# Optimization experiments

Hardware: AMD Instinct MI355X
Metric: run time of the kernel (lower is better)

The kernel has to match this reference:

```python
import jax, jax.numpy as jnp
import numpy as np

V, E, H, S, B, MAX_OOV = 50000, 256, 512, 500, 64, 50


def setup_inputs() -> dict:
    key = jax.random.key(0)
    ks = jax.random.split(key, 22)
    s = 0.02  # param init scale
    return {
        "input_token": jax.random.randint(ks[0], (B, 1), 0, V),
        "encoder_hidden_states": jax.random.normal(ks[1], (S, B, 2 * H), jnp.float32),
        "projected_encoder_hidden_states": jax.random.normal(ks[2], (S, B, H), jnp.float32),
        "src_mask": jnp.ones((B, S), dtype=bool),
        "prev_hidden": jax.random.normal(ks[3], (1, B, H), jnp.float32),
        "encoder_batch_extended_vocab": jax.random.randint(ks[4], (B, S), 0, V + MAX_OOV),
        "batch_max_oov": MAX_OOV,
        # learned parameters
        "emb": jax.random.normal(ks[5], (V, E), jnp.float32) * s,
        "attn_Wq": jax.random.normal(ks[6], (H, H), jnp.float32) * s,   # query_layer, no bias
        "attn_We": jax.random.normal(ks[7], (1, H), jnp.float32) * s,   # energy_layer, no bias
        "gru_Wih": jax.random.normal(ks[8], (3 * H, E + 2 * H), jnp.float32) * s,
        "gru_Whh": jax.random.normal(ks[9], (3 * H, H), jnp.float32) * s,
        "gru_bih": jax.random.normal(ks[10], (3 * H,), jnp.float32) * s,
        "gru_bhh": jax.random.normal(ks[11], (3 * H,), jnp.float32) * s,
        "lin_W": jax.random.normal(ks[12], (H, E + 3 * H), jnp.float32) * s,
        "lin_b": jax.random.normal(ks[13], (H,), jnp.float32) * s,
        "pg_W": jax.random.normal(ks[14], (1, E + 3 * H), jnp.float32) * s,
        "pg_b": jax.random.normal(ks[15], (1,), jnp.float32) * s,
        "out_W": jax.random.normal(ks[16], (V, H), jnp.float32) * s,
        "out_b": jax.random.normal(ks[17], (V,), jnp.float32) * s,
    }


def _forward(input_token, enc_h, proj_key, prev_hidden, ext_vocab, max_oov,
             emb, attn_Wq, attn_We, gru_Wih, gru_Whh, gru_bih, gru_bhh,
             lin_W, lin_b, pg_W, pg_b, out_W, out_b):
    b = input_token.shape[0]
    embed = jnp.transpose(emb[input_token], (1, 0, 2))  # [1,B,E]

    # Bahdanau attention (softmax over source dim 0; mask unused, as in source)
    q = jnp.einsum('tbh,oh->tbo', prev_hidden, attn_Wq)            # [1,B,H]
    scores = jnp.einsum('sbh,oh->sb', jnp.tanh(q + proj_key), attn_We)  # [S,B]
    alphas = jax.nn.softmax(scores, axis=0)                        # [S,B]
    context = jnp.einsum('sb,sbd->bd', alphas, enc_h)[None]        # [1,B,2H]
    attention_dist = alphas.T                                      # [B,S]

    # GRU cell (torch gate order: r, z, n)
    x = jnp.concatenate([embed, context], axis=2)[0]               # [B,E+2H]
    h = prev_hidden[0]                                             # [B,H]
    gi = x @ gru_Wih.T + gru_bih                                   # [B,3H]
    gh = h @ gru_Whh.T + gru_bhh
    i_r, i_z, i_n = jnp.split(gi, 3, axis=1)
    h_r, h_z, h_n = jnp.split(gh, 3, axis=1)
    r = jax.nn.sigmoid(i_r + h_r)
    z = jax.nn.sigmoid(i_z + h_z)
    n = jnp.tanh(i_n + r * h_n)
    h_new = (1.0 - z) * n + z * h                                  # [B,H]
    rnn_output = h_new[None]                                       # [1,B,H]

    concat = jnp.concatenate([embed, rnn_output, context], axis=2)  # [1,B,E+3H]
    p_gen = jax.nn.sigmoid(jnp.einsum('tbf,of->tbo', concat, pg_W) + pg_b)  # [1,B,1]
    lin = jnp.einsum('tbf,of->tbo', concat, lin_W) + lin_b          # [1,B,H]
    logits = jnp.einsum('tbh,vh->tbv', lin, out_W) + out_b          # [1,B,V]

    gen_prob = p_gen * jax.nn.softmax(logits, axis=2)               # [1,B,V]
    attn_prob = ((1.0 - p_gen) * attention_dist[None])[0]           # [B,S]

    ext = jnp.concatenate(
        [gen_prob, jnp.zeros((1, b, max_oov), gen_prob.dtype)], axis=2) + 1e-12  # [1,B,V+oov]
    rows = jnp.arange(b)[:, None]
    merged = ext.at[0, rows, ext_vocab].add(attn_prob)              # scatter_add over vocab dim
    output = jnp.log(merged)
    return output, h_new[None]


def reference(input_token, encoder_hidden_states, projected_encoder_hidden_states,
              src_mask, prev_hidden, encoder_batch_extended_vocab, batch_max_oov,
              emb, attn_Wq, attn_We, gru_Wih, gru_Whh, gru_bih, gru_bhh,
              lin_W, lin_b, pg_W, pg_b, out_W, out_b):
    return _forward(input_token, encoder_hidden_states, projected_encoder_hidden_states,
                    prev_hidden, encoder_batch_extended_vocab, batch_max_oov,
                    emb, attn_Wq, attn_We, gru_Wih, gru_Whh, gru_bih, gru_bhh,
                    lin_W, lin_b, pg_W, pg_b, out_W, out_b)
```

## Files before the change

### kernel.cpp

```cpp
#include <hip/hip_runtime.h>
#include <hip/hip_bf16.h>
#include <math.h>

namespace {
constexpr int V = 50000, E = 256, H = 512, S = 500, B = 64, OOVN = 50;
constexpr int VEXT = V + OOVN;
constexpr int CCAT = E + 3 * H;
constexpr int G3 = 3 * H;
constexpr int NLB = 391;

typedef __attribute__((ext_vector_type(8))) short short8;
typedef __attribute__((ext_vector_type(4))) float f32x4;

__device__ __forceinline__ float wsum(float v) {
#pragma unroll
  for (int off = 32; off > 0; off >>= 1) v += __shfl_xor(v, off, 64);
  return v;
}
__device__ __forceinline__ float sigmoidf(float x) { return 1.f / (1.f + __expf(-x)); }
__device__ __forceinline__ float fast_tanh(float x) {
  x = fminf(fmaxf(x, -15.f), 15.f);
  float e = __expf(2.f * x);
  return __fdividef(e - 1.f, e + 1.f);
}
__device__ __forceinline__ void smerge_s(float& m, float& l, float om, float ol) {
  float nm = fmaxf(m, om);
  if (nm == -INFINITY) { m = nm; return; }
  l = l * __expf(m - nm) + ol * __expf(om - nm);
  m = nm;
}
__device__ __forceinline__ short bf16_rn_s(float f) {
  __hip_bfloat16 h = __float2bfloat16(f);
  return __builtin_bit_cast(short, h);
}
__device__ __forceinline__ void hilo8(float4 a, float4 b, short8& hi, short8& lo) {
  float f[8] = {a.x, a.y, a.z, a.w, b.x, b.y, b.z, b.w};
#pragma unroll
  for (int i = 0; i < 8; ++i) {
    unsigned u = __float_as_uint(f[i]);
    hi[i] = (short)(u >> 16);
    lo[i] = bf16_rn_s(f[i] - __uint_as_float(u & 0xffff0000u));
  }
}

template <int KSTEPS>
__device__ __forceinline__ void gemm_core_f32(const float* __restrict__ X, int ldx,
                                              int xk0, const float* __restrict__ W,
                                              int ldw, int wk0, int n0, f32x4 acc[4]) {
  const int l = threadIdx.x & 63;
  const int r16 = l & 15, q16 = l >> 4;
#pragma unroll
  for (int t = 0; t < 4; ++t) acc[t] = (f32x4){0.f, 0.f, 0.f, 0.f};
  const float* wp = W + (size_t)(n0 + r16) * ldw + wk0 + q16 * 8;
  const float* xp[4];
#pragma unroll
  for (int t = 0; t < 4; ++t) xp[t] = X + (size_t)(t * 16 + r16) * ldx + xk0 + q16 * 8;
#pragma unroll
  for (int ks = 0; ks < KSTEPS; ++ks) {
    const int ko = ks * 32;
    float4 w0 = *reinterpret_cast<const float4*>(wp + ko);
    float4 w1 = *reinterpret_cast<const float4*>(wp + ko + 4);
    short8 whi, wlo;
    hilo8(w0, w1, whi, wlo);
#pragma unroll
    for (int t = 0; t < 4; ++t) {
      float4 x0 = *reinterpret_cast<const float4*>(xp[t] + ko);
      float4 x1 = *reinterpret_cast<const float4*>(xp[t] + ko + 4);
      short8 ah, al;
      hilo8(x0, x1, ah, al);
      acc[t] = __builtin_amdgcn_mfma_f32_16x16x32_bf16(ah, whi, acc[t], 0, 0, 0);
      acc[t] = __builtin_amdgcn_mfma_f32_16x16x32_bf16(al, whi, acc[t], 0, 0, 0);
      acc[t] = __builtin_amdgcn_mfma_f32_16x16x32_bf16(ah, wlo, acc[t], 0, 0, 0);
    }
  }
}
template <int KSTEPS>
__device__ __forceinline__ void gemm_store_f32(const float* X, int ldx, int xk0,
                                               const float* W, int ldw, int wk0, int n0,
                                               float* C, int ldc) {
  f32x4 acc[4];
  gemm_core_f32<KSTEPS>(X, ldx, xk0, W, ldw, wk0, n0, acc);
  const int l = threadIdx.x & 63;
  const int r16 = l & 15, q16 = l >> 4;
#pragma unroll
  for (int t = 0; t < 4; ++t)
#pragma unroll
    for (int r = 0; r < 4; ++r) {
      int row = t * 16 + q16 * 4 + r;
      C[(size_t)row * ldc + n0 + r16] = acc[t][r];
    }
}

__global__ void __launch_bounds__(256) k_head(const float* __restrict__ prevh,
                                              const float* __restrict__ Wq,
                                              const float* __restrict__ Whh,
                                              const int* __restrict__ tok,
                                              const float* __restrict__ emb,
                                              float* __restrict__ qpart,
                                              float* __restrict__ ghp,
                                              float* __restrict__ cc) {
  int gw = blockIdx.x * 4 + (threadIdx.x >> 6);
  if (gw < 128) {
    int c = gw >> 5, nt = gw & 31;
    gemm_store_f32<4>(prevh, H, c * 128, Wq, H, c * 128, nt * 16,
                      qpart + (size_t)c * 64 * H, H);
  } else if (gw < 320) {
    int w2 = gw - 128;
    int c = w2 / 96, nt = w2 % 96;
    gemm_store_f32<8>(prevh, H, c * 256, Whh, H, c * 256, nt * 16,
                      ghp + (size_t)c * 64 * G3, G3);
  } else {
    int idx = (gw - 320) * 64 + (threadIdx.x & 63);
    for (int i = idx; i < B * E; i += 1024) {
      int b = i >> 8, e = i & 255;
      cc[b * CCAT + e] = emb[(size_t)tok[b] * E + e];
    }
    for (int i = idx; i < B * 1024; i += 1024) {
      int b = i >> 10, col = i & 1023;
      cc[b * CCAT + 768 + col] = 0.f;
    }
  }
}

__global__ void k_scores(const float* __restrict__ qpart, const float* __restrict__ pk,
                         const float* __restrict__ We, float* __restrict__ scoresT) {
  int lane = threadIdx.x & 63;
  int gw = blockIdx.x * 4 + (threadIdx.x >> 6);
  int s = gw >> 6, b = gw & 63;
  const float* q0 = qpart + b * H + lane * 8;
  const float* kr = pk + ((size_t)s * B + b) * H + lane * 8;
  const float* er = We + lane * 8;
  float part = 0.f;
#pragma unroll
  for (int i = 0; i < 2; ++i) {
    float4 qa = *reinterpret_cast<const float4*>(q0 + i * 4);
    float4 qb = *reinterpret_cast<const float4*>(q0 + 64 * H + i * 4);
    float4 qc = *reinterpret_cast<const float4*>(q0 + 128 * H + i * 4);
    float4 qd = *reinterpret_cast<const float4*>(q0 + 192 * H + i * 4);
    float4 kv = *reinterpret_cast<const float4*>(kr + i * 4);
    float4 ev = *reinterpret_cast<const float4*>(er + i * 4);
    part += fast_tanh(qa.x + qb.x + qc.x + qd.x + kv.x) * ev.x +
            fast_tanh(qa.y + qb.y + qc.y + qd.y + kv.y) * ev.y +
            fast_tanh(qa.z + qb.z + qc.z + qd.z + kv.z) * ev.z +
            fast_tanh(qa.w + qb.w + qc.w + qd.w + kv.w) * ev.w;
  }
  part = wsum(part);
  if (lane == 0) scoresT[b * S + s] = part;
}

__global__ void k_softmax_s(const float* __restrict__ scoresT, float* __restrict__ alphasT) {
  int b = blockIdx.x, t = threadIdx.x;
  int w = t >> 6, lane = t & 63;
  __shared__ float rm[8], rl[8];
  float v = (t < S) ? scoresT[b * S + t] : -INFINITY;
  float m = v;
#pragma unroll
  for (int off = 32; off > 0; off >>= 1) m = fmaxf(m, __shfl_xor(m, off, 64));
  if (lane == 0) rm[w] = m;
  __syncthreads();
  float bm = rm[0];
#pragma unroll
  for (int i = 1; i < 8; ++i) bm = fmaxf(bm, rm[i]);
  float e = (t < S) ? __expf(v - bm) : 0.f;
  float sw = wsum(e);
  if (lane == 0) rl[w] = sw;
  __syncthreads();
  float tot = rl[0];
#pragma unroll
  for (int i = 1; i < 8; ++i) tot += rl[i];
  if (t < S) alphasT[b * S + t] = e / tot;
}

__global__ void k_ctx(const float* __restrict__ alphasT, const float* __restrict__ ench,
                      float* __restrict__ cc) {
  int x = blockIdx.x;
  int b = x >> 3, qd = (x >> 2) & 1 * 0 + ((x & 7) >> 1), sh = x & 1;
  int t = threadIdx.x;
  __shared__ float sa[250];
  if (t < 250) sa[t] = alphasT[b * S + sh * 250 + t];
  __syncthreads();
  const float* base = ench + ((size_t)(sh * 250) * B + b) * 1024 + qd * 256 + t;
  float a0 = 0.f, a1 = 0.f, a2 = 0.f, a3 = 0.f;
#pragma unroll 4
  for (int s = 0; s < 248; s += 4) {
    a0 += sa[s] * base[(size_t)s * (B * 1024)];
    a1 += sa[s + 1] * base[(size_t)(s + 1) * (B * 1024)];
    a2 += sa[s + 2] * base[(size_t)(s + 2) * (B * 1024)];
    a3 += sa[s + 3] * base[(size_t)(s + 3) * (B * 1024)];
  }
  a0 += sa[248] * base[(size_t)248 * (B * 1024)];
  a1 += sa[249] * base[(size_t)249 * (B * 1024)];
  atomicAdd(&cc[b * CCAT + 768 + qd * 256 + t], (a0 + a1) + (a2 + a3));
}

__global__ void __launch_bounds__(256) k_gemm_big(const float* __restrict__ cc,
                                                  const float* __restrict__ Wih,
                                                  const float* __restrict__ linW,
                                                  float* __restrict__ gip,
                                                  float* __restrict__ linpart) {
  int w = blockIdx.x * 4 + (threadIdx.x >> 6);
  if (w < 480) {
    int c = w / 96, nt = w % 96;
    int xk0 = (c == 0) ? 0 : 768 + (c - 1) * 256;
    gemm_store_f32<8>(cc, CCAT, xk0, Wih, 1280, c * 256, nt * 16,
                      gip + (size_t)c * 64 * G3, G3);
  } else {
    int w2 = w - 480;
    int c = w2 >> 5, nt = w2 & 31;
    int k0 = (c == 0) ? 0 : 768 + (c - 1) * 256;
    gemm_store_f32<8>(cc, CCAT, k0, linW, CCAT, k0, nt * 16,
                      linpart + (size_t)c * 64 * H, H);
  }
}

__global__ void k_gates(const float* __restrict__ gip, const float* __restrict__ ghp,
                        const float* __restrict__ bih, const float* __restrict__ bhh,
                        const float* __restrict__ prevh, const float* __restrict__ pgW,
                        const float* __restrict__ pgb, float* __restrict__ cc,
                        float* __restrict__ hout, float* __restrict__ pgsum) {
  int b = blockIdx.x, j = threadIdx.x;
  float ir = bih[j], iz = bih[512 + j], in_ = bih[1024 + j];
#pragma unroll
  for (int c = 0; c < 5; ++c) {
    const float* g = gip + (size_t)c * 64 * G3 + b * G3;
    ir += g[j]; iz += g[512 + j]; in_ += g[1024 + j];
  }
  float hr = bhh[j], hz = bhh[512 + j], hn = bhh[1024 + j];
#pragma unroll
  for (int c = 0; c < 2; ++c) {
    const float* g = ghp + (size_t)c * 64 * G3 + b * G3;
    hr += g[j]; hz += g[512 + j]; hn += g[1024 + j];
  }
  float r = sigmoidf(ir + hr);
  float z = sigmoidf(iz + hz);
  float n = fast_tanh(in_ + r * hn);
  float h = prevh[b * H + j];
  float hnew = (1.f - z) * n + z * h;
  hout[b * H + j] = hnew;
  cc[b * CCAT + E + j] = hnew;
  float acc = hnew * pgW[E + j];
  acc += cc[b * CCAT + 768 + j] * pgW[768 + j];
  acc += cc[b * CCAT + 1280 + j] * pgW[1280 + j];
  if (j < 256) acc += cc[b * CCAT + j] * pgW[j];
  acc = wsum(acc);
  __shared__ float sl[8];
  int w = j >> 6, lane = j & 63;
  if (lane == 0) sl[w] = acc;
  __syncthreads();
  if (j == 0) {
    float tot = pgb[0];
#pragma unroll
    for (int i = 0; i < 8; ++i) tot += sl[i];
    pgsum[b] = tot;
  }
}

__global__ void __launch_bounds__(256) k_linfin(const float* __restrict__ cc,
                                                const float* __restrict__ linW,
                                                const float* __restrict__ linpart,
                                                const float* __restrict__ linb,
                                                short* __restrict__ lh) {
  int w = blockIdx.x * 4 + (threadIdx.x >> 6);
  f32x4 acc[4];
  gemm_core_f32<16>(cc, CCAT, 256, linW, CCAT, 256, w * 16, acc);
  const int l = threadIdx.x & 63;
  const int r16 = l & 15, q16 = l >> 4;
  int col = w * 16 + r16;
  float bv = linb[col];
#pragma unroll
  for (int t = 0; t < 4; ++t)
#pragma unroll
    for (int r = 0; r < 4; ++r) {
      int row = t * 16 + q16 * 4 + r;
      float v = acc[t][r] + bv;
#pragma unroll
      for (int c = 0; c < 5; ++c) v += linpart[(size_t)c * 64 * H + row * H + col];
      lh[row * H + col] = bf16_rn_s(v);
    }
}

__global__ void __launch_bounds__(512) k_gemm_logits(
    const short* __restrict__ lh, const float* __restrict__ outW,
    const float* __restrict__ outb, float* __restrict__ logits,
    float* __restrict__ pm, float* __restrict__ pl) {
  __shared__ __align__(16) short xs[64 * 512];
  __shared__ float pml[8][64][2];
  char* xb = reinterpret_cast<char*>(xs);
  int tid = threadIdx.x;
#pragma unroll
  for (int k = 0; k < 8; ++k) {
    int m = k * 512 + tid;
    int row = m >> 6;
    short8 v = *reinterpret_cast<const short8*>(lh + (size_t)m * 8);
    int byte = (m * 16) ^ ((row & 7) << 4);
    *reinterpret_cast<short8*>(xb + byte) = v;
  }
  __syncthreads();
  const int l = tid & 63;
  const int r16 = l & 15, q16 = l >> 4;
  const int wid = tid >> 6;
  const int waveId = blockIdx.x * 8 + wid;
  const bool active = waveId < V / 16;
  if (active) {
    const int n0 = waveId * 16;
    f32x4 acc[4];
#pragma unroll
    for (int t = 0; t < 4; ++t) acc[t] = (f32x4){0.f, 0.f, 0.f, 0.f};
    const float* wp = outW + (size_t)(n0 + r16) * H + q16 * 8;
    int arow[4], aswz[4];
#pragma unroll
    for (int t = 0; t < 4; ++t) {
      int row = t * 16 + r16;
      arow[t] = row * 1024 + q16 * 16;
      aswz[t] = (row & 7) << 4;
    }
#pragma unroll
    for (int ks = 0; ks < 16; ++ks) {
      float4 w0 = *reinterpret_cast<const float4*>(wp + ks * 32);
      float4 w1 = *reinterpret_cast<const float4*>(wp + ks * 32 + 4);
      short8 wh;
      wh[0] = bf16_rn_s(w0.x); wh[1] = bf16_rn_s(w0.y);
      wh[2] = bf16_rn_s(w0.z); wh[3] = bf16_rn_s(w0.w);
      wh[4] = bf16_rn_s(w1.x); wh[5] = bf16_rn_s(w1.y);
      wh[6] = bf16_rn_s(w1.z); wh[7] = bf16_rn_s(w1.w);
#pragma unroll
      for (int t = 0; t < 4; ++t) {
        short8 a = *reinterpret_cast<const short8*>(xb + ((arow[t] + ks * 64) ^ aswz[t]));
        acc[t] = __builtin_amdgcn_mfma_f32_16x16x32_bf16(a, wh, acc[t], 0, 0, 0);
      }
    }
    float bv = outb[n0 + r16];
#pragma unroll
    for (int t = 0; t < 4; ++t)
#pragma unroll
      for (int r = 0; r < 4; ++r) {
        float y = acc[t][r] + bv;
        int row = t * 16 + q16 * 4 + r;
        logits[(size_t)row * V + n0 + r16] = y;
        float m = y;
#pragma unroll
        for (int off = 8; off > 0; off >>= 1) m = fmaxf(m, __shfl_xor(m, off, 64));
        float e = __expf(y - m);
#pragma unroll
        for (int off = 8; off > 0; off >>= 1) e += __shfl_xor(e, off, 64);
        if (r16 == 0) { pml[wid][row][0] = m; pml[wid][row][1] = e; }
      }
  } else if (r16 == 0) {
#pragma unroll
    for (int t = 0; t < 4; ++t)
#pragma unroll
      for (int r = 0; r < 4; ++r) {
        int row = t * 16 + q16 * 4 + r;
        pml[wid][row][0] = -INFINITY;
        pml[wid][row][1] = 0.f;
      }
  }
  __syncthreads();
  if (tid < 64) {
    float m = pml[0][tid][0], lv = pml[0][tid][1];
#pragma unroll
    for (int i = 1; i < 8; ++i) smerge_s(m, lv, pml[i][tid][0], pml[i][tid][1]);
    pm[blockIdx.x * 64 + tid] = m;
    pl[blockIdx.x * 64 + tid] = lv;
  }
}

__global__ void k_final(const float* __restrict__ logits, const float* __restrict__ pm,
                        const float* __restrict__ pl, const float* __restrict__ pgsum,
                        const int* __restrict__ extv, const float* __restrict__ alphasT,
                        float* __restrict__ out) {
  int b = blockIdx.x, c = blockIdx.y, t = threadIdx.x;
  __shared__ float sp_[5056];
  __shared__ float rm[4], rl[4];
  float m = -INFINITY, lv = 0.f;
  for (int i = t; i < NLB; i += 256) smerge_s(m, lv, pm[i * 64 + b], pl[i * 64 + b]);
#pragma unroll
  for (int off = 32; off > 0; off >>= 1) {
    float om = __shfl_xor(m, off, 64), ol = __shfl_xor(lv, off, 64);
    smerge_s(m, lv, om, ol);
  }
  int w = t >> 6, lane = t & 63;
  if (lane == 0) { rm[w] = m; rl[w] = lv; }
  __syncthreads();
  m = rm[0]; lv = rl[0];
#pragma unroll
  for (int i = 1; i < 4; ++i) smerge_s(m, lv, rm[i], rl[i]);
  float pg = sigmoidf(pgsum[b]);
  float scale = pg / lv;
  const int base = c * 5000;
  const int len = (c == 9) ? 5050 : 5000;
  const float* lr = logits + (size_t)b * V + base;
  for (int i = t; i < len; i += 256)
    sp_[i] = (i < 5000) ? scale * __expf(lr[i] - m) + 1e-12f : 1e-12f;
  __syncthreads();
  float wgt = 1.f - pg;
  for (int s = t; s < S; s += 256) {
    int idx = extv[b * S + s] - base;
    if ((unsigned)idx < (unsigned)len) atomicAdd(&sp_[idx], wgt * alphasT[b * S + s]);
  }
  __syncthreads();
  float* orow = out + (size_t)b * VEXT + base;
  for (int i = t; i < len; i += 256) orow[i] = __logf(sp_[i]);
}
}

extern "C" void kernel_launch(void* const* d_in, const int* in_sizes, int n_in,
                              void* d_out, int out_size, void* d_ws, size_t ws_size,
                              hipStream_t stream) {
  const int*   tok   = (const int*)d_in[0];
  const float* ench  = (const float*)d_in[1];
  const float* pk    = (const float*)d_in[2];
  const float* prevh = (const float*)d_in[4];
  const int*   extv  = (const int*)d_in[5];
  const float* emb   = (const float*)d_in[7];
  const float* Wq    = (const float*)d_in[8];
  const float* We    = (const float*)d_in[9];
  const float* Wih   = (const float*)d_in[10];
  const float* Whh   = (const float*)d_in[11];
  const float* bih   = (const float*)d_in[12];
  const float* bhh   = (const float*)d_in[13];
  const float* linW  = (const float*)d_in[14];
  const float* linb  = (const float*)d_in[15];
  const float* pgW   = (const float*)d_in[16];
  const float* pgb   = (const float*)d_in[17];
  const float* outW  = (const float*)d_in[18];
  const float* outb  = (const float*)d_in[19];

  float* out = (float*)d_out;
  float* ws = (float*)d_ws;

  float* qpart   = ws;
  float* scoresT = qpart + 131072;
  float* alphasT = scoresT + 32000;
  float* cc      = alphasT + 32000;
  float* gip     = cc + 114688;
  float* ghp     = gip + 491520;
  float* linpart = ghp + 196608;
  float* pgsum   = linpart + 163840;
  float* logits  = pgsum + 64;
  float* pm      = logits + 3200000;
  float* pl      = pm + 25024;
  short* lh      = (short*)(pl + 25024);
  float* hout    = out + (size_t)B * VEXT;

  k_head<<<dim3(84), dim3(256), 0, stream>>>(prevh, Wq, Whh, tok, emb, qpart, ghp, cc);
  k_scores<<<dim3(8000), dim3(256), 0, stream>>>(qpart, pk, We, scoresT);
  k_softmax_s<<<dim3(B), dim3(512), 0, stream>>>(scoresT, alphasT);
  k_ctx<<<dim3(512), dim3(256), 0, stream>>>(alphasT, ench, cc);
  k_gemm_big<<<dim3(160), dim3(256), 0, stream>>>(cc, Wih, linW, gip, linpart);
  k_gates<<<dim3(B), dim3(512), 0, stream>>>(gip, ghp, bih, bhh, prevh, pgW, pgb, cc,
                                             hout, pgsum);
  k_linfin<<<dim3(8), dim3(256), 0, stream>>>(cc, linW, linpart, linb, lh);
  k_gemm_logits<<<dim3(NLB), dim3(512), 0, stream>>>(lh, outW, outb, logits, pm, pl);
  k_final<<<dim3(B, 10), dim3(256), 0, stream>>>(logits, pm, pl, pgsum, extv, alphasT, out);
}
```

Baseline: 149.9 us.

## Fuse softmax into context kernel, move Whh GEMM, store logits as bf16

```diff
diff --git a/kernel.cpp b/kernel.cpp
--- a/kernel.cpp
+++ b/kernel.cpp
@@ -32,6 +32,9 @@
 __device__ __forceinline__ short bf16_rn_s(float f) {
   __hip_bfloat16 h = __float2bfloat16(f);
   return __builtin_bit_cast(short, h);
+}
+__device__ __forceinline__ float bf16s_to_f(unsigned short u) {
+  return __uint_as_float(((unsigned)u) << 16);
 }
 __device__ __forceinline__ void hilo8(float4 a, float4 b, short8& hi, short8& lo) {
   float f[8] = {a.x, a.y, a.z, a.w, b.x, b.y, b.z, b.w};
@@ -93,24 +96,17 @@
 
 __global__ void __launch_bounds__(256) k_head(const float* __restrict__ prevh,
                                               const float* __restrict__ Wq,
-                                              const float* __restrict__ Whh,
                                               const int* __restrict__ tok,
                                               const float* __restrict__ emb,
                                               float* __restrict__ qpart,
-                                              float* __restrict__ ghp,
                                               float* __restrict__ cc) {
   int gw = blockIdx.x * 4 + (threadIdx.x >> 6);
   if (gw < 128) {
     int c = gw >> 5, nt = gw & 31;
     gemm_store_f32<4>(prevh, H, c * 128, Wq, H, c * 128, nt * 16,
                       qpart + (size_t)c * 64 * H, H);
-  } else if (gw < 320) {
-    int w2 = gw - 128;
-    int c = w2 / 96, nt = w2 % 96;
-    gemm_store_f32<8>(prevh, H, c * 256, Whh, H, c * 256, nt * 16,
-                      ghp + (size_t)c * 64 * G3, G3);
   } else {
-    int idx = (gw - 320) * 64 + (threadIdx.x & 63);
+    int idx = (gw - 128) * 64 + (threadIdx.x & 63);
     for (int i = idx; i < B * E; i += 1024) {
       int b = i >> 8, e = i & 255;
       cc[b * CCAT + e] = emb[(size_t)tok[b] * E + e];
@@ -148,36 +144,40 @@
   if (lane == 0) scoresT[b * S + s] = part;
 }
 
-__global__ void k_softmax_s(const float* __restrict__ scoresT, float* __restrict__ alphasT) {
-  int b = blockIdx.x, t = threadIdx.x;
+__global__ void k_ctx(const float* __restrict__ scoresT, const float* __restrict__ ench,
+                      float* __restrict__ cc, float* __restrict__ alphasT) {
+  int x = blockIdx.x;
+  int b = x >> 3, qd = (x >> 1) & 3, sh = x & 1;
+  int t = threadIdx.x;
+  __shared__ float sa[250];
+  __shared__ float rm[4], rl[4];
   int w = t >> 6, lane = t & 63;
-  __shared__ float rm[8], rl[8];
-  float v = (t < S) ? scoresT[b * S + t] : -INFINITY;
-  float m = v;
+  float v0 = scoresT[b * S + t];
+  float v1 = (t + 256 < S) ? scoresT[b * S + t + 256] : -INFINITY;
+  float m = fmaxf(v0, v1);
 #pragma unroll
   for (int off = 32; off > 0; off >>= 1) m = fmaxf(m, __shfl_xor(m, off, 64));
   if (lane == 0) rm[w] = m;
   __syncthreads();
-  float bm = rm[0];
-#pragma unroll
-  for (int i = 1; i < 8; ++i) bm = fmaxf(bm, rm[i]);
-  float e = (t < S) ? __expf(v - bm) : 0.f;
-  float sw = wsum(e);
+  float bm = fmaxf(fmaxf(rm[0], rm[1]), fmaxf(rm[2], rm[3]));
+  float e0 = __expf(v0 - bm);
+  float e1 = (t + 256 < S) ? __expf(v1 - bm) : 0.f;
+  float sw = wsum(e0 + e1);
   if (lane == 0) rl[w] = sw;
   __syncthreads();
-  float tot = rl[0];
-#pragma unroll
-  for (int i = 1; i < 8; ++i) tot += rl[i];
-  if (t < S) alphasT[b * S + t] = e / tot;
-}
-
-__global__ void k_ctx(const float* __restrict__ alphasT, const float* __restrict__ ench,
-                      float* __restrict__ cc) {
-  int x = blockIdx.x;
-  int b = x >> 3, qd = (x >> 2) & 1 * 0 + ((x & 7) >> 1), sh = x & 1;
-  int t = threadIdx.x;
-  __shared__ float sa[250];
-  if (t < 250) sa[t] = alphasT[b * S + sh * 250 + t];
+  float tot = rl[0] + rl[1] + rl[2] + rl[3];
+  float a0v = e0 / tot;
+  float a1v = e1 / tot;
+  if (sh == 0) {
+    if (t < 250) sa[t] = a0v;
+  } else {
+    if (t >= 250) sa[t - 250] = a0v;
+    if (t + 256 < S) sa[t + 6] = a1v;
+  }
+  if (qd == 0) {
+    if (sh == 0) alphasT[b * S + t] = a0v;
+    else if (t + 256 < S) alphasT[b * S + t + 256] = a1v;
+  }
   __syncthreads();
   const float* base = ench + ((size_t)(sh * 250) * B + b) * 1024 + qd * 256 + t;
   float a0 = 0.f, a1 = 0.f, a2 = 0.f, a3 = 0.f;
@@ -194,22 +194,30 @@
 }
 
 __global__ void __launch_bounds__(256) k_gemm_big(const float* __restrict__ cc,
+                                                  const float* __restrict__ prevh,
                                                   const float* __restrict__ Wih,
+                                                  const float* __restrict__ Whh,
                                                   const float* __restrict__ linW,
                                                   float* __restrict__ gip,
-                                                  float* __restrict__ linpart) {
+                                                  float* __restrict__ linpart,
+                                                  float* __restrict__ ghp) {
   int w = blockIdx.x * 4 + (threadIdx.x >> 6);
   if (w < 480) {
     int c = w / 96, nt = w % 96;
     int xk0 = (c == 0) ? 0 : 768 + (c - 1) * 256;
     gemm_store_f32<8>(cc, CCAT, xk0, Wih, 1280, c * 256, nt * 16,
                       gip + (size_t)c * 64 * G3, G3);
-  } else {
+  } else if (w < 640) {
     int w2 = w - 480;
     int c = w2 >> 5, nt = w2 & 31;
     int k0 = (c == 0) ? 0 : 768 + (c - 1) * 256;
     gemm_store_f32<8>(cc, CCAT, k0, linW, CCAT, k0, nt * 16,
                       linpart + (size_t)c * 64 * H, H);
+  } else {
+    int w2 = w - 640;
+    int c = w2 / 96, nt = w2 % 96;
+    gemm_store_f32<8>(prevh, H, c * 256, Whh, H, c * 256, nt * 16,
+                      ghp + (size_t)c * 64 * G3, G3);
   }
 }
 
@@ -281,7 +289,7 @@
 
 __global__ void __launch_bounds__(512) k_gemm_logits(
     const short* __restrict__ lh, const float* __restrict__ outW,
-    const float* __restrict__ outb, float* __restrict__ logits,
+    const float* __restrict__ outb, unsigned short* __restrict__ logitsb,
     float* __restrict__ pm, float* __restrict__ pl) {
   __shared__ __align__(16) short xs[64 * 512];
   __shared__ float pml[8][64][2];
@@ -336,7 +344,7 @@
       for (int r = 0; r < 4; ++r) {
         float y = acc[t][r] + bv;
         int row = t * 16 + q16 * 4 + r;
-        logits[(size_t)row * V + n0 + r16] = y;
+        logitsb[(size_t)row * V + n0 + r16] = (unsigned short)bf16_rn_s(y);
         float m = y;
 #pragma unroll
         for (int off = 8; off > 0; off >>= 1) m = fmaxf(m, __shfl_xor(m, off, 64));
@@ -365,10 +373,10 @@
   }
 }
 
-__global__ void k_final(const float* __restrict__ logits, const float* __restrict__ pm,
-                        const float* __restrict__ pl, const float* __restrict__ pgsum,
-                        const int* __restrict__ extv, const float* __restrict__ alphasT,
-                        float* __restrict__ out) {
+__global__ void k_final(const unsigned short* __restrict__ logitsb,
+                        const float* __restrict__ pm, const float* __restrict__ pl,
+                        const float* __restrict__ pgsum, const int* __restrict__ extv,
+                        const float* __restrict__ alphasT, float* __restrict__ out) {
   int b = blockIdx.x, c = blockIdx.y, t = threadIdx.x;
   __shared__ float sp_[5056];
   __shared__ float rm[4], rl[4];
@@ -389,9 +397,9 @@
   float scale = pg / lv;
   const int base = c * 5000;
   const int len = (c == 9) ? 5050 : 5000;
-  const float* lr = logits + (size_t)b * V + base;
+  const unsigned short* lr = logitsb + (size_t)b * V + base;
   for (int i = t; i < len; i += 256)
-    sp_[i] = (i < 5000) ? scale * __expf(lr[i] - m) + 1e-12f : 1e-12f;
+    sp_[i] = (i < 5000) ? scale * __expf(bf16s_to_f(lr[i]) - m) + 1e-12f : 1e-12f;
   __syncthreads();
   float wgt = 1.f - pg;
   for (int s = t; s < S; s += 256) {
@@ -437,20 +445,20 @@
   float* ghp     = gip + 491520;
   float* linpart = ghp + 196608;
   float* pgsum   = linpart + 163840;
-  float* logits  = pgsum + 64;
-  float* pm      = logits + 3200000;
+  float* pm      = pgsum + 64;
   float* pl      = pm + 25024;
-  short* lh      = (short*)(pl + 25024);
+  unsigned short* logitsb = (unsigned short*)(pl + 25024);
+  short* lh      = (short*)(logitsb + (size_t)B * V);
   float* hout    = out + (size_t)B * VEXT;
 
-  k_head<<<dim3(84), dim3(256), 0, stream>>>(prevh, Wq, Whh, tok, emb, qpart, ghp, cc);
+  k_head<<<dim3(36), dim3(256), 0, stream>>>(prevh, Wq, tok, emb, qpart, cc);
   k_scores<<<dim3(8000), dim3(256), 0, stream>>>(qpart, pk, We, scoresT);
-  k_softmax_s<<<dim3(B), dim3(512), 0, stream>>>(scoresT, alphasT);
-  k_ctx<<<dim3(512), dim3(256), 0, stream>>>(alphasT, ench, cc);
-  k_gemm_big<<<dim3(160), dim3(256), 0, stream>>>(cc, Wih, linW, gip, linpart);
+  k_ctx<<<dim3(512), dim3(256), 0, stream>>>(scoresT, ench, cc, alphasT);
+  k_gemm_big<<<dim3(208), dim3(256), 0, stream>>>(cc, prevh, Wih, Whh, linW, gip,
+                                                  linpart, ghp);
   k_gates<<<dim3(B), dim3(512), 0, stream>>>(gip, ghp, bih, bhh, prevh, pgW, pgb, cc,
                                              hout, pgsum);
   k_linfin<<<dim3(8), dim3(256), 0, stream>>>(cc, linW, linpart, linb, lh);
-  k_gemm_logits<<<dim3(NLB), dim3(512), 0, stream>>>(lh, outW, outb, logits, pm, pl);
-  k_final<<<dim3(B, 10), dim3(256), 0, stream>>>(logits, pm, pl, pgsum, extv, alphasT, out);
-}
+  k_gemm_logits<<<dim3(NLB), dim3(512), 0, stream>>>(lh, outW, outb, logitsb, pm, pl);
+  k_final<<<dim3(B, 10), dim3(256), 0, stream>>>(logitsb, pm, pl, pgsum, extv, alphasT, out);
+}
```

Result: slower. 154.0 us (+2.7%).

## Split context reduction into partial-sum pass and store logits as bf16

Applied to the files above, without the earlier changes.

```diff
diff --git a/kernel.cpp b/kernel.cpp
--- a/kernel.cpp
+++ b/kernel.cpp
@@ -32,6 +32,9 @@
 __device__ __forceinline__ short bf16_rn_s(float f) {
   __hip_bfloat16 h = __float2bfloat16(f);
   return __builtin_bit_cast(short, h);
+}
+__device__ __forceinline__ float bf16s_to_f(unsigned short u) {
+  return __uint_as_float(((unsigned)u) << 16);
 }
 __device__ __forceinline__ void hilo8(float4 a, float4 b, short8& hi, short8& lo) {
   float f[8] = {a.x, a.y, a.z, a.w, b.x, b.y, b.z, b.w};
@@ -115,10 +118,6 @@
       int b = i >> 8, e = i & 255;
       cc[b * CCAT + e] = emb[(size_t)tok[b] * E + e];
     }
-    for (int i = idx; i < B * 1024; i += 1024) {
-      int b = i >> 10, col = i & 1023;
-      cc[b * CCAT + 768 + col] = 0.f;
-    }
   }
 }
 
@@ -171,26 +170,40 @@
   if (t < S) alphasT[b * S + t] = e / tot;
 }
 
-__global__ void k_ctx(const float* __restrict__ alphasT, const float* __restrict__ ench,
-                      float* __restrict__ cc) {
+__global__ void __launch_bounds__(256) k_ctxp(const float* __restrict__ alphasT,
+                                              const float* __restrict__ ench,
+                                              float* __restrict__ ctxp) {
   int x = blockIdx.x;
-  int b = x >> 3, qd = (x >> 2) & 1 * 0 + ((x & 7) >> 1), sh = x & 1;
+  int b = x >> 5, ch = x & 31;
   int t = threadIdx.x;
-  __shared__ float sa[250];
-  if (t < 250) sa[t] = alphasT[b * S + sh * 250 + t];
-  __syncthreads();
-  const float* base = ench + ((size_t)(sh * 250) * B + b) * 1024 + qd * 256 + t;
-  float a0 = 0.f, a1 = 0.f, a2 = 0.f, a3 = 0.f;
-#pragma unroll 4
-  for (int s = 0; s < 248; s += 4) {
-    a0 += sa[s] * base[(size_t)s * (B * 1024)];
-    a1 += sa[s + 1] * base[(size_t)(s + 1) * (B * 1024)];
-    a2 += sa[s + 2] * base[(size_t)(s + 2) * (B * 1024)];
-    a3 += sa[s + 3] * base[(size_t)(s + 3) * (B * 1024)];
-  }
-  a0 += sa[248] * base[(size_t)248 * (B * 1024)];
-  a1 += sa[249] * base[(size_t)249 * (B * 1024)];
-  atomicAdd(&cc[b * CCAT + 768 + qd * 256 + t], (a0 + a1) + (a2 + a3));
+  int s0 = ch * 16;
+  int cnt = (s0 + 16 <= S) ? 16 : (S - s0);
+  float sa[16];
+#pragma unroll
+  for (int j = 0; j < 16; ++j) sa[j] = (j < cnt) ? alphasT[b * S + s0 + j] : 0.f;
+  const float* eb = ench + ((size_t)s0 * B + b) * 1024 + t * 4;
+  float ax = 0.f, ay = 0.f, az = 0.f, aw = 0.f;
+#pragma unroll
+  for (int j = 0; j < 16; ++j) {
+    if (j < cnt) {
+      float4 v = *reinterpret_cast<const float4*>(eb + (size_t)j * (B * 1024));
+      ax += sa[j] * v.x; ay += sa[j] * v.y; az += sa[j] * v.z; aw += sa[j] * v.w;
+    }
+  }
+  float4 o; o.x = ax; o.y = ay; o.z = az; o.w = aw;
+  *reinterpret_cast<float4*>(ctxp + (size_t)x * 1024 + t * 4) = o;
+}
+
+__global__ void k_ctx2(const float* __restrict__ ctxp, float* __restrict__ cc) {
+  int b = blockIdx.x, t = threadIdx.x;
+  float ax = 0.f, ay = 0.f, az = 0.f, aw = 0.f;
+#pragma unroll
+  for (int ch = 0; ch < 32; ++ch) {
+    float4 v = *reinterpret_cast<const float4*>(ctxp + (size_t)((b << 5) | ch) * 1024 + t * 4);
+    ax += v.x; ay += v.y; az += v.z; aw += v.w;
+  }
+  float4 o; o.x = ax; o.y = ay; o.z = az; o.w = aw;
+  *reinterpret_cast<float4*>(cc + b * CCAT + 768 + t * 4) = o;
 }
 
 __global__ void __launch_bounds__(256) k_gemm_big(const float* __restrict__ cc,
@@ -281,7 +294,7 @@
 
 __global__ void __launch_bounds__(512) k_gemm_logits(
     const short* __restrict__ lh, const float* __restrict__ outW,
-    const float* __restrict__ outb, float* __restrict__ logits,
+    const float* __restrict__ outb, unsigned short* __restrict__ logitsb,
     float* __restrict__ pm, float* __restrict__ pl) {
   __shared__ __align__(16) short xs[64 * 512];
   __shared__ float pml[8][64][2];
@@ -336,7 +349,7 @@
       for (int r = 0; r < 4; ++r) {
         float y = acc[t][r] + bv;
         int row = t * 16 + q16 * 4 + r;
-        logits[(size_t)row * V + n0 + r16] = y;
+        logitsb[(size_t)row * V + n0 + r16] = (unsigned short)bf16_rn_s(y);
         float m = y;
 #pragma unroll
         for (int off = 8; off > 0; off >>= 1) m = fmaxf(m, __shfl_xor(m, off, 64));
@@ -365,10 +378,10 @@
   }
 }
 
-__global__ void k_final(const float* __restrict__ logits, const float* __restrict__ pm,
-                        const float* __restrict__ pl, const float* __restrict__ pgsum,
-                        const int* __restrict__ extv, const float* __restrict__ alphasT,
-                        float* __restrict__ out) {
+__global__ void k_final(const unsigned short* __restrict__ logitsb,
+                        const float* __restrict__ pm, const float* __restrict__ pl,
+                        const float* __restrict__ pgsum, const int* __restrict__ extv,
+                        const float* __restrict__ alphasT, float* __restrict__ out) {
   int b = blockIdx.x, c = blockIdx.y, t = threadIdx.x;
   __shared__ float sp_[5056];
   __shared__ float rm[4], rl[4];
@@ -389,9 +402,9 @@
   float scale = pg / lv;
   const int base = c * 5000;
   const int len = (c == 9) ? 5050 : 5000;
-  const float* lr = logits + (size_t)b * V + base;
+  const unsigned short* lr = logitsb + (size_t)b * V + base;
   for (int i = t; i < len; i += 256)
-    sp_[i] = (i < 5000) ? scale * __expf(lr[i] - m) + 1e-12f : 1e-12f;
+    sp_[i] = (i < 5000) ? scale * __expf(bf16s_to_f(lr[i]) - m) + 1e-12f : 1e-12f;
   __syncthreads();
   float wgt = 1.f - pg;
   for (int s = t; s < S; s += 256) {
@@ -432,25 +445,27 @@
   float* qpart   = ws;
   float* scoresT = qpart + 131072;
   float* alphasT = scoresT + 32000;
-  float* cc      = alphasT + 32000;
+  float* ctxp    = alphasT + 32000;
+  float* cc      = ctxp + 2097152;
   float* gip     = cc + 114688;
   float* ghp     = gip + 491520;
   float* linpart = ghp + 196608;
   float* pgsum   = linpart + 163840;
-  float* logits  = pgsum + 64;
-  float* pm      = logits + 3200000;
+  float* pm      = pgsum + 64;
   float* pl      = pm + 25024;
-  short* lh      = (short*)(pl + 25024);
+  unsigned short* logitsb = (unsigned short*)(pl + 25024);
+  short* lh      = (short*)(logitsb + (size_t)B * V);
   float* hout    = out + (size_t)B * VEXT;
 
   k_head<<<dim3(84), dim3(256), 0, stream>>>(prevh, Wq, Whh, tok, emb, qpart, ghp, cc);
   k_scores<<<dim3(8000), dim3(256), 0, stream>>>(qpart, pk, We, scoresT);
   k_softmax_s<<<dim3(B), dim3(512), 0, stream>>>(scoresT, alphasT);
-  k_ctx<<<dim3(512), dim3(256), 0, stream>>>(alphasT, ench, cc);
+  k_ctxp<<<dim3(2048), dim3(256), 0, stream>>>(alphasT, ench, ctxp);
+  k_ctx2<<<dim3(B), dim3(256), 0, stream>>>(ctxp, cc);
   k_gemm_big<<<dim3(160), dim3(256), 0, stream>>>(cc, Wih, linW, gip, linpart);
   k_gates<<<dim3(B), dim3(512), 0, stream>>>(gip, ghp, bih, bhh, prevh, pgW, pgb, cc,
                                              hout, pgsum);
   k_linfin<<<dim3(8), dim3(256), 0, stream>>>(cc, linW, linpart, linb, lh);
-  k_gemm_logits<<<dim3(NLB), dim3(512), 0, stream>>>(lh, outW, outb, logits, pm, pl);
-  k_final<<<dim3(B, 10), dim3(256), 0, stream>>>(logits, pm, pl, pgsum, extv, alphasT, out);
-}
+  k_gemm_logits<<<dim3(NLB), dim3(512), 0, stream>>>(lh, outW, outb, logitsb, pm, pl);
+  k_final<<<dim3(B, 10), dim3(256), 0, stream>>>(logitsb, pm, pl, pgsum, extv, alphasT, out);
+}
```

After: 160.5 us. 7.0% more time.
